# Kernel optimization log

Hardware: AMD Instinct MI355X
Metric: run time of the kernel (lower is better)

Reference implementation:

```python
import jax, jax.numpy as jnp
import numpy as np

B, K, H, W, N = 256, 16, 64, 64, 1024   # batch, channels (n_ch), grid H/W, sampled sites
F_IN = 9 * K - 1                         # 3x3 neighborhood * K channels, minus center channel


def setup_inputs() -> dict:
    key = jax.random.key(0)
    ks = jax.random.split(key, 8)
    z_int = jax.random.randint(ks[0], (B, K, H, W), 0, 16, dtype=jnp.int32)
    bs = jax.random.randint(ks[1], (N,), 0, K, dtype=jnp.int32)
    ii = jax.random.randint(ks[2], (N,), 0, H, dtype=jnp.int32)
    jj = jax.random.randint(ks[3], (N,), 0, W, dtype=jnp.int32)
    W1 = jax.random.normal(ks[4], (F_IN, 128), dtype=jnp.float32) * 0.05
    b1 = jnp.zeros((128,), dtype=jnp.float32)
    W2 = jax.random.normal(ks[5], (128, 16), dtype=jnp.float32) * 0.05
    b2 = jnp.zeros((16,), dtype=jnp.float32)
    return {"z_int": z_int, "bs": bs, "ii": ii, "jj": jj,
            "W1": W1, "b1": b1, "W2": W2, "b2": b2}


def _gather_ctx(z_f, bs, ii, jj):
    # Faithful to get_context ordering: loops di, dj (each in [-1,0,1]) then b,
    # skipping (di==0, dj==0, b==bi). Flattened skip position = 4*K + bi.
    off = jnp.array([-1, 0, 1], dtype=jnp.int32)
    di = jnp.repeat(off, 3)          # [9]
    dj = jnp.tile(off, 3)            # [9]
    ni = (ii[:, None] + di[None, :]) % H   # [N, 9] toroidal wrap
    nj = (jj[:, None] + dj[None, :]) % W   # [N, 9]
    ctx = z_f[:, :, ni, nj]                # [B, K, N, 9]
    ctx = jnp.transpose(ctx, (2, 0, 3, 1)).reshape(N, B, 9 * K)  # [N, B, 9K], (di,dj) major then b
    drop = 4 * K + bs                      # [N] center-channel flat index
    idx = jnp.arange(F_IN, dtype=jnp.int32)
    keep = idx[None, :] + (idx[None, :] >= drop[:, None]).astype(jnp.int32)  # [N, F_IN]
    return jax.vmap(lambda c, k: c[:, k])(ctx, keep)  # [N, B, F_IN]


def reference(z_int, bs, ii, jj, W1, b1, W2, b2):
    z_f = z_int.astype(jnp.float32) / 15.0
    ctx = _gather_ctx(z_f, bs, ii, jj)                 # [N, B, 9K-1]
    h = jax.nn.relu(jnp.einsum('nbf,fh->nbh', ctx, W1) + b1)
    logits = jnp.einsum('nbh,hc->nbc', h, W2) + b2     # [N, B, 16]
    pred = jnp.argmax(logits, axis=-1)                 # [N, B]
    tgt = z_int[:, bs, ii, jj].T                       # [N, B]
    rate = jnp.mean((pred != tgt).astype(jnp.float32)) # np.mean of per-site mean == global mean
    return rate
```

## Files before the change

kernel.cpp:

```cpp
#include <hip/hip_runtime.h>
#include <stdint.h>

#define NB 1024
#define BB 256
#define KK 16
#define HH 64
#define WW 64
#define F_FULL 144
#define HDIM 128
#define CDIM 16
#define KPAD 160
#define APITCH 168
#define HPITCH 136
#define ABYTES (64 * APITCH * 2)

typedef __bf16 bf16x8 __attribute__((ext_vector_type(8)));
typedef float f32x4 __attribute__((ext_vector_type(4)));

#define W1T_OFF 256
#define W1T_BYTES (16 * HDIM * KPAD * 2)
#define W2B_OFF (W1T_OFF + W1T_BYTES)
#define W2B_BYTES (CDIM * HDIM * 2)
#define ZT_OFF (W2B_OFF + W2B_BYTES)

__device__ __forceinline__ unsigned short bf16_bits(float v) {
    __bf16 b = (__bf16)v;
    return __builtin_bit_cast(unsigned short, b);
}

#define TP 144
__global__ __launch_bounds__(256) void prep_kernel(
    const int* __restrict__ z, const float* __restrict__ W1,
    const float* __restrict__ W2, uint8_t* __restrict__ zt,
    unsigned short* __restrict__ W1t, unsigned short* __restrict__ W2b,
    int* __restrict__ counters) {
    int bid = blockIdx.x;
    int t = threadIdx.x;
    if (bid < 4096) {
        __shared__ uint8_t tile[32 * TP];
        int bx = bid & 127;
        int by = bid >> 7;
        int c0 = bx * 32, r0 = by * 128;
#pragma unroll
        for (int i = 0; i < 4; ++i) {
            int lin = i * 256 + t;
            int c = lin & 31;
            int rq = lin >> 5;
            uchar4 v;
            v.x = (uint8_t)z[(size_t)(r0 + rq * 4 + 0) * 4096 + c0 + c];
            v.y = (uint8_t)z[(size_t)(r0 + rq * 4 + 1) * 4096 + c0 + c];
            v.z = (uint8_t)z[(size_t)(r0 + rq * 4 + 2) * 4096 + c0 + c];
            v.w = (uint8_t)z[(size_t)(r0 + rq * 4 + 3) * 4096 + c0 + c];
            *(uchar4*)(tile + c * TP + rq * 4) = v;
        }
        __syncthreads();
        int cy = t >> 3, rx = t & 7;
        uint4 v = *(const uint4*)(tile + cy * TP + rx * 16);
        *(uint4*)(zt + (size_t)(c0 + cy) * 4096 + r0 + rx * 16) = v;
    } else if (bid < 5376) {
        int idx = (bid - 4096) * 256 + t;
        int k = idx % KPAD;
        int h = (idx / KPAD) % HDIM;
        int s = idx / (KPAD * HDIM);
        int drop = 4 * KK + s;
        float val = 0.0f;
        if (k < F_FULL && k != drop) {
            int src = k - (k > drop ? 1 : 0);
            val = W1[src * HDIM + h];
        }
        W1t[idx] = bf16_bits(val);
    } else {
        int idx = (bid - 5376) * 256 + t;
        if (idx < CDIM * HDIM) {
            int k = idx % HDIM;
            int c = idx / HDIM;
            W2b[idx] = bf16_bits(W2[k * CDIM + c]);
        }
        if (bid == 5376 && t == 0) counters[0] = 0;
    }
}

__global__ __launch_bounds__(256, 3) void main_kernel(
    const uint8_t* __restrict__ zt, const unsigned short* __restrict__ W1t,
    const float* __restrict__ b1, const unsigned short* __restrict__ W2b,
    const float* __restrict__ b2, const int* __restrict__ bs,
    const int* __restrict__ ii, const int* __restrict__ jj,
    int* __restrict__ counters) {
    __shared__ __align__(16) unsigned char smem[2 * ABYTES + 64 * 17 * 4];
    unsigned short* sA0 = (unsigned short*)smem;
    unsigned short* sA1 = (unsigned short*)(smem + ABYTES);
    float* slg = (float*)(smem + 2 * ABYTES);

    int t = threadIdx.x;
    int n = blockIdx.x;
    int wave = t >> 6, lane = t & 63;
    int l15 = lane & 15, l4 = lane >> 4;

    int in_ = ii[n], jn = jj[n], sn = bs[n];

    const unsigned short* w1s = W1t + (size_t)sn * (HDIM * KPAD);
    int n0 = wave * 32;
    bf16x8 Bf[2][5];
#pragma unroll
    for (int nt = 0; nt < 2; ++nt)
#pragma unroll
        for (int ks = 0; ks < 5; ++ks)
            Bf[nt][ks] = *(const bf16x8*)(w1s + (n0 + nt * 16 + l15) * KPAD + ks * 32 + l4 * 8);
    bf16x8 Bf2[4];
#pragma unroll
    for (int ks = 0; ks < 4; ++ks)
        Bf2[ks] = *(const bf16x8*)(W2b + l15 * HDIM + ks * 32 + l4 * 8);
    float b1v0 = b1[n0 + l15], b1v1 = b1[n0 + 16 + l15];
    float b2v = b2[l15];

    if (t < 192) {
        int b = t / 3, part = t % 3;
        *(uint4*)(sA0 + b * APITCH + F_FULL + part * 8) = make_uint4(0, 0, 0, 0);
        *(uint4*)(sA1 + b * APITCH + F_FULL + part * 8) = make_uint4(0, 0, 0, 0);
    }

    uint4 g0, g1, g2;
    auto gload = [&](int tile) {
        int b = (t & 63) + tile * 64;
        int p0 = t >> 6;
        int ni0 = (in_ + p0 / 3 - 1) & (HH - 1);
        int nj0 = (jn + p0 % 3 - 1) & (WW - 1);
        g0 = *(const uint4*)(zt + (((size_t)(ni0 * WW + nj0) * BB + b) << 4));
        int p1 = p0 + 4;
        int ni1 = (in_ + p1 / 3 - 1) & (HH - 1);
        int nj1 = (jn + p1 % 3 - 1) & (WW - 1);
        g1 = *(const uint4*)(zt + (((size_t)(ni1 * WW + nj1) * BB + b) << 4));
        if (t < 64) {
            int ni2 = (in_ + 1) & (HH - 1);
            int nj2 = (jn + 1) & (WW - 1);
            g2 = *(const uint4*)(zt + (((size_t)(ni2 * WW + nj2) * BB + b) << 4));
        }
    };
    auto gwrite = [&](unsigned short* dst) {
        int b = t & 63;
        int p0 = t >> 6;
        auto conv = [&](uint4 raw, int p) {
            const uint8_t* bytes = (const uint8_t*)&raw;
            union { __bf16 h[16]; uint4 q[2]; } u;
#pragma unroll
            for (int k = 0; k < 16; ++k)
                u.h[k] = (__bf16)((float)bytes[k] * (1.0f / 15.0f));
            uint4* d = (uint4*)(dst + b * APITCH + p * 16);
            d[0] = u.q[0];
            d[1] = u.q[1];
        };
        conv(g0, p0);
        conv(g1, p0 + 4);
        if (t < 64) conv(g2, 8);
    };

    gload(0);
    gwrite(sA0);
    int local_err = 0;

    for (int tile = 0; tile < 4; ++tile) {
        unsigned short* sA = (tile & 1) ? sA1 : sA0;
        unsigned short* sH = sA;
        unsigned short* sAnext = (tile & 1) ? sA0 : sA1;

        if (tile < 3) gload(tile + 1);
        __syncthreads();

        f32x4 acc[4][2] = {};
#pragma unroll
        for (int mt = 0; mt < 4; ++mt) {
            bf16x8 Af[5];
#pragma unroll
            for (int ks = 0; ks < 5; ++ks)
                Af[ks] = *(const bf16x8*)(sA + (mt * 16 + l15) * APITCH + ks * 32 + l4 * 8);
#pragma unroll
            for (int ks = 0; ks < 5; ++ks) {
                acc[mt][0] = __builtin_amdgcn_mfma_f32_16x16x32_bf16(Af[ks], Bf[0][ks], acc[mt][0], 0, 0, 0);
                acc[mt][1] = __builtin_amdgcn_mfma_f32_16x16x32_bf16(Af[ks], Bf[1][ks], acc[mt][1], 0, 0, 0);
            }
        }
        __syncthreads();

#pragma unroll
        for (int mt = 0; mt < 4; ++mt)
#pragma unroll
            for (int nt = 0; nt < 2; ++nt) {
                float bv = nt ? b1v1 : b1v0;
                int hcol = n0 + nt * 16 + l15;
#pragma unroll
                for (int r = 0; r < 4; ++r) {
                    int b = mt * 16 + l4 * 4 + r;
                    float v = fmaxf(acc[mt][nt][r] + bv, 0.0f);
                    sH[b * HPITCH + hcol] = bf16_bits(v);
                }
            }
        __syncthreads();

        f32x4 acc2 = {};
#pragma unroll
        for (int ks = 0; ks < 4; ++ks) {
            bf16x8 Af = *(const bf16x8*)(sH + (wave * 16 + l15) * HPITCH + ks * 32 + l4 * 8);
            acc2 = __builtin_amdgcn_mfma_f32_16x16x32_bf16(Af, Bf2[ks], acc2, 0, 0, 0);
        }
#pragma unroll
        for (int r = 0; r < 4; ++r) {
            int b = wave * 16 + l4 * 4 + r;
            slg[b * 17 + l15] = acc2[r] + b2v;
        }
        __syncthreads();

        if (t < 64) {
            float best = slg[t * 17];
            int pi = 0;
#pragma unroll
            for (int c = 1; c < CDIM; ++c) {
                float v = slg[t * 17 + c];
                if (v > best) { best = v; pi = c; }
            }
            int bglob = tile * 64 + t;
            int tgt = zt[(((size_t)(in_ * WW + jn) * BB + bglob) << 4) + sn];
            unsigned long long m = __ballot(pi != tgt);
            if (t == 0) local_err += (int)__popcll(m);
        }
        if (tile < 3) gwrite(sAnext);
    }

    if (t == 0) atomicAdd(&counters[0], local_err);
}

__global__ void finalize_kernel(const int* __restrict__ counters, float* __restrict__ out) {
    out[0] = (float)(counters[0]) / (float)(NB * BB);
}

extern "C" void kernel_launch(void* const* d_in, const int* in_sizes, int n_in,
                              void* d_out, int out_size, void* d_ws, size_t ws_size,
                              hipStream_t stream) {
    const int* z = (const int*)d_in[0];
    const int* bs = (const int*)d_in[1];
    const int* ii = (const int*)d_in[2];
    const int* jj = (const int*)d_in[3];
    const float* W1 = (const float*)d_in[4];
    const float* b1 = (const float*)d_in[5];
    const float* W2 = (const float*)d_in[6];
    const float* b2 = (const float*)d_in[7];
    float* out = (float*)d_out;

    uint8_t* ws = (uint8_t*)d_ws;
    int* counters = (int*)ws;
    unsigned short* W1t = (unsigned short*)(ws + W1T_OFF);
    unsigned short* W2b = (unsigned short*)(ws + W2B_OFF);
    uint8_t* zt = ws + ZT_OFF;

    prep_kernel<<<5384, 256, 0, stream>>>(z, W1, W2, zt, W1t, W2b, counters);
    main_kernel<<<NB, 256, 0, stream>>>(zt, W1t, b1, W2b, b2, bs, ii, jj, counters);
    finalize_kernel<<<1, 1, 0, stream>>>(counters, out);
}
```

Before: 135.3 us.

## Prefetch all neighbor tiles up front, shuffle-based argmax, spread error counters

New measurement: 145.0 us. +7.2%, slower.

```diff
diff --git a/kernel.cpp b/kernel.cpp
--- a/kernel.cpp
+++ b/kernel.cpp
@@ -13,11 +13,12 @@
 #define APITCH 168
 #define HPITCH 136
 #define ABYTES (64 * APITCH * 2)
+#define NCTR 128
 
 typedef __bf16 bf16x8 __attribute__((ext_vector_type(8)));
 typedef float f32x4 __attribute__((ext_vector_type(4)));
 
-#define W1T_OFF 256
+#define W1T_OFF 1024
 #define W1T_BYTES (16 * HDIM * KPAD * 2)
 #define W2B_OFF (W1T_OFF + W1T_BYTES)
 #define W2B_BYTES (CDIM * HDIM * 2)
@@ -76,7 +77,7 @@
             int c = idx / HDIM;
             W2b[idx] = bf16_bits(W2[k * CDIM + c]);
         }
-        if (bid == 5376 && t == 0) counters[0] = 0;
+        if (bid == 5376 && t < NCTR) counters[t] = 0;
     }
 }
 
@@ -86,10 +87,9 @@
     const float* __restrict__ b2, const int* __restrict__ bs,
     const int* __restrict__ ii, const int* __restrict__ jj,
     int* __restrict__ counters) {
-    __shared__ __align__(16) unsigned char smem[2 * ABYTES + 64 * 17 * 4];
+    __shared__ __align__(16) unsigned char smem[2 * ABYTES + 1024];
     unsigned short* sA0 = (unsigned short*)smem;
     unsigned short* sA1 = (unsigned short*)(smem + ABYTES);
-    float* slg = (float*)(smem + 2 * ABYTES);
 
     int t = threadIdx.x;
     int n = blockIdx.x;
@@ -98,6 +98,36 @@
 
     int in_ = ii[n], jn = jj[n], sn = bs[n];
 
+    {
+        const uint8_t* src = zt + ((size_t)n << 14) + t * 16;
+#pragma unroll
+        for (int k = 0; k < 4; ++k)
+            __builtin_amdgcn_global_load_lds(
+                (const __attribute__((address_space(1))) void*)(src + (k << 12)),
+                (__attribute__((address_space(3))) void*)(smem + 2 * ABYTES), 16, 0, 0);
+    }
+
+    int p0 = t >> 6;
+    int ni0 = (in_ + p0 / 3 - 1) & (HH - 1);
+    int nj0 = (jn + p0 % 3 - 1) & (WW - 1);
+    size_t base0 = ((size_t)(ni0 * WW + nj0) * BB) << 4;
+    int p1 = p0 + 4;
+    int ni1 = (in_ + p1 / 3 - 1) & (HH - 1);
+    int nj1 = (jn + p1 % 3 - 1) & (WW - 1);
+    size_t base1 = ((size_t)(ni1 * WW + nj1) * BB) << 4;
+    int ni2 = (in_ + 1) & (HH - 1);
+    int nj2 = (jn + 1) & (WW - 1);
+    size_t base2 = ((size_t)(ni2 * WW + nj2) * BB) << 4;
+
+    uint4 ga[4], gb[4], gc[4];
+#pragma unroll
+    for (int tl = 0; tl < 3; ++tl) {
+        size_t boff = (size_t)((t & 63) + tl * 64) << 4;
+        ga[tl] = *(const uint4*)(zt + base0 + boff);
+        gb[tl] = *(const uint4*)(zt + base1 + boff);
+        if (t < 64) gc[tl] = *(const uint4*)(zt + base2 + boff);
+    }
+
     const unsigned short* w1s = W1t + (size_t)sn * (HDIM * KPAD);
     int n0 = wave * 32;
     bf16x8 Bf[2][5];
@@ -119,26 +149,8 @@
         *(uint4*)(sA1 + b * APITCH + F_FULL + part * 8) = make_uint4(0, 0, 0, 0);
     }
 
-    uint4 g0, g1, g2;
-    auto gload = [&](int tile) {
-        int b = (t & 63) + tile * 64;
-        int p0 = t >> 6;
-        int ni0 = (in_ + p0 / 3 - 1) & (HH - 1);
-        int nj0 = (jn + p0 % 3 - 1) & (WW - 1);
-        g0 = *(const uint4*)(zt + (((size_t)(ni0 * WW + nj0) * BB + b) << 4));
-        int p1 = p0 + 4;
-        int ni1 = (in_ + p1 / 3 - 1) & (HH - 1);
-        int nj1 = (jn + p1 % 3 - 1) & (WW - 1);
-        g1 = *(const uint4*)(zt + (((size_t)(ni1 * WW + nj1) * BB + b) << 4));
-        if (t < 64) {
-            int ni2 = (in_ + 1) & (HH - 1);
-            int nj2 = (jn + 1) & (WW - 1);
-            g2 = *(const uint4*)(zt + (((size_t)(ni2 * WW + nj2) * BB + b) << 4));
-        }
-    };
-    auto gwrite = [&](unsigned short* dst) {
+    auto gwrite = [&](uint4 A, uint4 B, uint4 C, unsigned short* dst) {
         int b = t & 63;
-        int p0 = t >> 6;
         auto conv = [&](uint4 raw, int p) {
             const uint8_t* bytes = (const uint8_t*)&raw;
             union { __bf16 h[16]; uint4 q[2]; } u;
@@ -149,21 +161,19 @@
             d[0] = u.q[0];
             d[1] = u.q[1];
         };
-        conv(g0, p0);
-        conv(g1, p0 + 4);
-        if (t < 64) conv(g2, 8);
+        conv(A, p0);
+        conv(B, p0 + 4);
+        if (t < 64) conv(C, 8);
     };
 
-    gload(0);
-    gwrite(sA0);
-    int local_err = 0;
+    gwrite(ga[0], gb[0], gc[0], sA0);
+
+    int err = 0;
+    size_t tbase = ((size_t)(in_ * WW + jn) * BB) << 4;
 
     for (int tile = 0; tile < 4; ++tile) {
         unsigned short* sA = (tile & 1) ? sA1 : sA0;
         unsigned short* sH = sA;
-        unsigned short* sAnext = (tile & 1) ? sA0 : sA1;
-
-        if (tile < 3) gload(tile + 1);
         __syncthreads();
 
         f32x4 acc[4][2] = {};
@@ -202,34 +212,45 @@
             bf16x8 Af = *(const bf16x8*)(sH + (wave * 16 + l15) * HPITCH + ks * 32 + l4 * 8);
             acc2 = __builtin_amdgcn_mfma_f32_16x16x32_bf16(Af, Bf2[ks], acc2, 0, 0, 0);
         }
+
 #pragma unroll
         for (int r = 0; r < 4; ++r) {
-            int b = wave * 16 + l4 * 4 + r;
-            slg[b * 17 + l15] = acc2[r] + b2v;
-        }
-        __syncthreads();
-
-        if (t < 64) {
-            float best = slg[t * 17];
-            int pi = 0;
-#pragma unroll
-            for (int c = 1; c < CDIM; ++c) {
-                float v = slg[t * 17 + c];
-                if (v > best) { best = v; pi = c; }
+            float v = acc2[r] + b2v;
+            int idx = l15;
+#pragma unroll
+            for (int m = 1; m < 16; m <<= 1) {
+                float ov = __shfl_xor(v, m);
+                int oi = __shfl_xor(idx, m);
+                if (ov > v || (ov == v && oi < idx)) { v = ov; idx = oi; }
             }
-            int bglob = tile * 64 + t;
-            int tgt = zt[(((size_t)(in_ * WW + jn) * BB + bglob) << 4) + sn];
-            unsigned long long m = __ballot(pi != tgt);
-            if (t == 0) local_err += (int)__popcll(m);
-        }
-        if (tile < 3) gwrite(sAnext);
-    }
-
-    if (t == 0) atomicAdd(&counters[0], local_err);
+            int bg = tile * 64 + wave * 16 + l4 * 4 + r;
+            int tgt = zt[tbase + ((size_t)bg << 4) + sn];
+            unsigned long long mm = __ballot(l15 == 0 && idx != tgt);
+            err += (int)__popcll(mm);
+        }
+
+        if (tile == 0) {
+            gwrite(ga[1], gb[1], gc[1], sA1);
+            size_t boff = (size_t)((t & 63) + 192) << 4;
+            ga[3] = *(const uint4*)(zt + base0 + boff);
+            gb[3] = *(const uint4*)(zt + base1 + boff);
+            if (t < 64) gc[3] = *(const uint4*)(zt + base2 + boff);
+        } else if (tile == 1) {
+            gwrite(ga[2], gb[2], gc[2], sA0);
+        } else if (tile == 2) {
+            gwrite(ga[3], gb[3], gc[3], sA1);
+        }
+    }
+
+    if (lane == 0) atomicAdd(&counters[n & (NCTR - 1)], err);
 }
 
 __global__ void finalize_kernel(const int* __restrict__ counters, float* __restrict__ out) {
-    out[0] = (float)(counters[0]) / (float)(NB * BB);
+    int t = threadIdx.x;
+    int s = counters[t] + counters[t + 64];
+#pragma unroll
+    for (int m = 32; m; m >>= 1) s += __shfl_down(s, m);
+    if (t == 0) out[0] = (float)s / (float)(NB * BB);
 }
 
 extern "C" void kernel_launch(void* const* d_in, const int* in_sizes, int n_in,
@@ -253,5 +274,5 @@
 
     prep_kernel<<<5384, 256, 0, stream>>>(z, W1, W2, zt, W1t, W2b, counters);
     main_kernel<<<NB, 256, 0, stream>>>(zt, W1t, b1, W2b, b2, bs, ii, jj, counters);
-    finalize_kernel<<<1, 1, 0, stream>>>(counters, out);
-}
+    finalize_kernel<<<1, 1 * 64, 0, stream>>>(counters, out);
+}
```
